# Performance work log

Hardware: AMD Instinct MI355X
Metric: run time of the kernel (lower is better)

Reference implementation:

```python
import jax, jax.numpy as jnp
import numpy as np

S_MUL, V_MUL = 32, 16          # 32x0e + 16x1o
NODE_DIM = S_MUL + 3 * V_MUL   # 80
LATENT = 128
INV_SQRT3 = 1.0 / np.sqrt(3.0)          # wigner 3j (1,1,0) / (0,1,1) / (1,0,1) factor
C_SCALAR = np.float32(1.0 / np.sqrt(48.0))   # path_norm 'element': fan into 0e = 32*1 + 16*1
C_VECTOR = np.float32(np.sqrt(3.0 / 48.0))   # irrep dim 3 / fan 48 for 1o output


def setup_inputs() -> dict:
    rng = np.random.default_rng(0)
    B, n_atoms, radius = 2048, 32, 5.0
    N = B * n_atoms
    # atoms uniform in a 10A cube -> ~300 edges per 32-atom graph at r=5
    pos_g = rng.uniform(0.0, 10.0, size=(B, n_atoms, 3)).astype(np.float32)
    diff = pos_g[:, :, None, :] - pos_g[:, None, :, :]
    d2 = (diff * diff).sum(-1)
    mask = (d2 <= radius * radius) & (d2 > 0.0)   # same predicate as build_radius_graph
    b_idx, i_idx, j_idx = np.nonzero(mask)
    edge_index = np.stack([b_idx * n_atoms + i_idx, b_idx * n_atoms + j_idx]).astype(np.int32)
    pos = pos_g.reshape(N, 3)
    z = rng.integers(0, 100, size=N).astype(np.int32)
    batch = np.repeat(np.arange(B, dtype=np.int32), n_atoms)
    L = 3  # num_layers

    def w(*shape, scale=1.0):
        return jnp.asarray((rng.standard_normal(shape) * scale).astype(np.float32))

    return dict(
        pos=jnp.asarray(pos), z=jnp.asarray(z), batch=jnp.asarray(batch),
        edge_index=jnp.asarray(edge_index), num_graphs=B,
        emb=w(100, S_MUL),                      # nn.Embedding(100, 32) ~ N(0,1)
        W_s2n=w(S_MUL, S_MUL),                  # e3nn Linear 32x0e -> 32x0e path
        W1=w(L, S_MUL, S_MUL),                  # tp path 0e x 0e -> 0e
        W2=w(L, S_MUL, V_MUL),                  # tp path 0e x 1o -> 1o
        W3=w(L, V_MUL, V_MUL),                  # tp path 1o x 0e -> 1o
        W4=w(L, V_MUL, S_MUL),                  # tp path 1o x 1o -> 0e
        Ws=w(L, S_MUL, S_MUL),                  # e3nn Linear scalar block
        Wv=w(L, V_MUL, V_MUL),                  # e3nn Linear vector block
        Wr1=w(NODE_DIM, 256, scale=1.0 / np.sqrt(NODE_DIM)), br1=jnp.zeros((256,), jnp.float32),
        Wr2=w(256, LATENT, scale=1.0 / np.sqrt(256.0)), br2=jnp.zeros((LATENT,), jnp.float32),
    )


def _forward(pos, emb, W_s2n, W1, W2, W3, W4, Ws, Wv, Wr1, br1, Wr2, br2,
             z, batch, edge_index, num_graphs):
    N = pos.shape[0]
    src, dst = edge_index[0], edge_index[1]
    # atom embedding -> node irreps (only 0e->0e path exists; vectors start at 0)
    s = (emb[z] @ W_s2n) * np.float32(1.0 / np.sqrt(S_MUL))   # (N, 32)
    v = jnp.zeros((N, V_MUL, 3), pos.dtype)                   # (N, 16, 3)
    # spherical harmonics, normalize=True, 'component': Y0 = 1, Y1 = sqrt(3) * r_hat
    rij = pos[dst] - pos[src]                                 # (E, 3)
    sh1 = np.float32(np.sqrt(3.0)) * rij / jnp.linalg.norm(rij, axis=-1, keepdims=True)
    for l in range(W1.shape[0]):
        ss, vs = s[src], v[src]                               # gather (E,32), (E,16,3)
        # FullyConnectedTensorProduct(node, sh, node), uvw weights, sh0 == 1
        m_s = C_SCALAR * (jnp.einsum('eu,uw->ew', ss, W1[l])
                          + INV_SQRT3 * jnp.einsum('eui,ei,uw->ew', vs, sh1, W4[l]))
        m_v = (C_VECTOR * INV_SQRT3) * (jnp.einsum('eu,ei,uw->ewi', ss, sh1, W2[l])
                                        + jnp.einsum('eui,uw->ewi', vs, W3[l]))
        a_s = jax.ops.segment_sum(m_s, dst, num_segments=N)   # index_add_ scatter
        a_v = jax.ops.segment_sum(m_v, dst, num_segments=N)
        # e3nn Linear (per-irrep block, 1/sqrt(fan_in)) then relu on FULL feature (as in source)
        h_s = jax.nn.relu((a_s @ Ws[l]) * np.float32(1.0 / np.sqrt(S_MUL)))
        h_v = jax.nn.relu(jnp.einsum('nvi,vw->nwi', a_v, Wv[l]) * np.float32(1.0 / np.sqrt(V_MUL)))
        s, v = s + h_s, v + h_v                               # residual
    x = jnp.concatenate([s, v.reshape(N, V_MUL * 3)], axis=-1)  # (N, 80)
    hg = jax.ops.segment_sum(x, batch, num_segments=num_graphs) # sum-pool per graph
    return jax.nn.relu(hg @ Wr1 + br1) @ Wr2 + br2              # (B, latent)


def reference(pos, emb, W_s2n, W1, W2, W3, W4, Ws, Wv, Wr1, br1, Wr2, br2,
              z, batch, edge_index, num_graphs):
    return _forward(pos, emb, W_s2n, W1, W2, W3, W4, Ws, Wv, Wr1, br1, Wr2, br2,
                    z, batch, edge_index, num_graphs)
```

## Files before the change

### kernel.cpp

```cpp
#include <hip/hip_runtime.h>
#include <math.h>

typedef __attribute__((ext_vector_type(8))) short bf16x8;
typedef __attribute__((ext_vector_type(4))) float f32x4;

#define SQRT3F     1.7320508075688772f
#define SCALE_T    0.17677669529663687f
#define SCALE_M1   0.025515518153991442f
#define SCALE_M2   0.014731391274719739f
#define SCALE_M34  0.036084391824351615f

#define FSTR 40
#define ASTR 72

__device__ __forceinline__ ushort f2bf(float f) {
    union { float f; unsigned u; } v; v.f = f;
    unsigned u = v.u;
    return (ushort)((u + 0x7FFFu + ((u >> 16) & 1u)) >> 16);
}
__device__ __forceinline__ float bf2f(ushort h) {
    union { unsigned u; float f; } v; v.u = ((unsigned)h) << 16;
    return v.f;
}
__device__ __forceinline__ f32x4 mfma(bf16x8 a, bf16x8 b, f32x4 c) {
    return __builtin_amdgcn_mfma_f32_16x16x32_bf16(a, b, c, 0, 0, 0);
}
__device__ __forceinline__ void storeAgg(ushort* AG, f32x4 t, int u0, int n) {
    uint2 u;
    u.x = f2bf(t[0]) | ((unsigned)f2bf(t[1]) << 16);
    u.y = f2bf(t[2]) | ((unsigned)f2bf(t[3]) << 16);
    *(uint2*)&AG[n*ASTR + u0] = u;
}
__device__ __forceinline__ void rmw4(ushort* F, int c, int n0, f32x4 h) {
    uint2* p = (uint2*)&F[c*FSTR + n0];
    uint2 o = *p;
    float f0 = bf2f((ushort)(o.x      )) + fmaxf(h[0], 0.f);
    float f1 = bf2f((ushort)(o.x >> 16)) + fmaxf(h[1], 0.f);
    float f2 = bf2f((ushort)(o.y      )) + fmaxf(h[2], 0.f);
    float f3 = bf2f((ushort)(o.y >> 16)) + fmaxf(h[3], 0.f);
    uint2 w;
    w.x = f2bf(f0) | ((unsigned)f2bf(f1) << 16);
    w.y = f2bf(f2) | ((unsigned)f2bf(f3) << 16);
    *p = w;
}

__global__ void prep_kernel(const float* __restrict__ emb,
                            const float* __restrict__ W_s2n,
                            const float* __restrict__ W1, const float* __restrict__ W2,
                            const float* __restrict__ W3, const float* __restrict__ W4,
                            const float* __restrict__ Ws, const float* __restrict__ Wv,
                            ushort* __restrict__ Tbf, ushort* __restrict__ Mbf)
{
    int idx = blockIdx.x * blockDim.x + threadIdx.x;
    if (idx < 3200) {
        int r = idx >> 5, c = idx & 31;
        float acc = 0.f;
        for (int k = 0; k < 32; ++k) acc += emb[r*32 + k] * W_s2n[k*32 + c];
        Tbf[idx] = f2bf(acc * SCALE_T);
        return;
    }
    idx -= 3200;
    if (idx < 3*48*64) {
        int lyr = idx / 3072, rem = idx % 3072;
        int row = rem >> 6, u = rem & 63;
        float val = 0.f;
        if (row < 32) {
            int w = row;
            if (u < 32) {
                float a = 0.f;
                for (int k = 0; k < 32; ++k)
                    a += W1[lyr*1024 + u*32 + k] * Ws[lyr*1024 + k*32 + w];
                val = a * SCALE_M1;
            } else if (u < 48) {
                int uu = u - 32; float a = 0.f;
                for (int k = 0; k < 32; ++k)
                    a += W4[lyr*512 + uu*32 + k] * Ws[lyr*1024 + k*32 + w];
                val = a * SCALE_M2;
            }
        } else {
            int w = row - 32;
            if (u < 32) {
                float a = 0.f;
                for (int k = 0; k < 16; ++k)
                    a += W2[lyr*512 + u*16 + k] * Wv[lyr*256 + k*16 + w];
                val = a * SCALE_M34;
            } else if (u < 48) {
                int uu = u - 32; float a = 0.f;
                for (int k = 0; k < 16; ++k)
                    a += W3[lyr*256 + uu*16 + k] * Wv[lyr*256 + k*16 + w];
                val = a * SCALE_M34;
            }
        }
        Mbf[lyr*3072 + row*64 + u] = f2bf(val);
    }
}

__global__ __launch_bounds__(256)
void gnn_kernel(const float* __restrict__ pos, const int* __restrict__ z,
                const ushort* __restrict__ Tbf, const ushort* __restrict__ Mbf,
                const float* __restrict__ Wr1, const float* __restrict__ br1,
                const float* __restrict__ Wr2, const float* __restrict__ br2,
                float* __restrict__ out, int B)
{
    __shared__ __align__(16) char smem[45312];
    ushort* featA = (ushort*)smem;
    ushort* aggA  = (ushort*)(smem + 25600);
    float*  hgl   = (float*)(smem + 44032);
    float*  h1    = (float*)aggA;
    float*  red   = ((float*)aggA) + 1024;

    const int tid = threadIdx.x;
    const int wv = tid >> 6, l = tid & 63;
    const int g  = blockIdx.x*4 + wv;
    ushort* F  = featA + wv*80*FSTR;
    ushort* AG = aggA  + wv*32*ASTR;

    for (int i = l; i < 32*(ASTR/2); i += 64) ((uint*)AG)[i] = 0;
    for (int i = l; i < 48*(FSTR/2); i += 64) ((uint*)(F + 32*FSTR))[i] = 0;

    {
        int n = l & 31, h = l >> 5;
        int zg = z[g*32 + n];
        uint4 t0 = *(const uint4*)(Tbf + zg*32 + h*16);
        uint4 t1 = *(const uint4*)(Tbf + zg*32 + h*16 + 8);
        unsigned ua[8] = {t0.x, t0.y, t0.z, t0.w, t1.x, t1.y, t1.z, t1.w};
        #pragma unroll
        for (int q = 0; q < 8; ++q) {
            F[(h*16 + 2*q    )*FSTR + n] = (ushort)ua[q];
            F[(h*16 + 2*q + 1)*FSTR + n] = (ushort)(ua[q] >> 16);
        }
    }

    const int ln = l & 15, kq = l >> 4;
    bf16x8 adjf[4][2];
    {
        const int k0 = kq*8;
        #pragma unroll
        for (int nt = 0; nt < 2; ++nt) {
            int ng = g*32 + nt*16 + ln;
            float px = pos[3*ng], py = pos[3*ng+1], pz = pos[3*ng+2];
            union { bf16x8 v; ushort s[8]; } o[4];
            #pragma unroll
            for (int jj = 0; jj < 8; ++jj) {
                int j = g*32 + k0 + jj;
                float dx = __fsub_rn(px, pos[3*j]);
                float dy = __fsub_rn(py, pos[3*j+1]);
                float dz = __fsub_rn(pz, pos[3*j+2]);
                float d2 = __fadd_rn(__fadd_rn(__fmul_rn(dx,dx), __fmul_rn(dy,dy)),
                                     __fmul_rn(dz,dz));
                bool on = (d2 <= 25.0f) && (d2 > 0.0f);
                float rinv = on ? rsqrtf(d2) * SQRT3F : 0.f;
                o[0].s[jj] = on ? (ushort)0x3F80 : (ushort)0;
                o[1].s[jj] = f2bf(dx * rinv);
                o[2].s[jj] = f2bf(dy * rinv);
                o[3].s[jj] = f2bf(dz * rinv);
            }
            #pragma unroll
            for (int w = 0; w < 4; ++w) adjf[w][nt] = o[w].v;
        }
    }

    const f32x4 z4 = {0.f, 0.f, 0.f, 0.f};

    for (int lay = 0; lay < 3; ++lay) {
        const ushort* Mg = Mbf + lay*3072;
        bf16x8 fs0 = *(const bf16x8*)&F[(     ln)*FSTR + kq*8];
        bf16x8 fs1 = *(const bf16x8*)&F[(16 + ln)*FSTR + kq*8];
        bf16x8 fv0 = *(const bf16x8*)&F[(32 + ln)*FSTR + kq*8];
        bf16x8 fv1 = *(const bf16x8*)&F[(48 + ln)*FSTR + kq*8];
        bf16x8 fv2 = *(const bf16x8*)&F[(64 + ln)*FSTR + kq*8];
        bf16x8 bmS0[2], bmS1[2], bmV[2];
        #pragma unroll
        for (int kc = 0; kc < 2; ++kc) {
            bmS0[kc] = *(const bf16x8*)&Mg[(     ln)*64 + kc*32 + kq*8];
            bmS1[kc] = *(const bf16x8*)&Mg[(16 + ln)*64 + kc*32 + kq*8];
            bmV [kc] = *(const bf16x8*)&Mg[(32 + ln)*64 + kc*32 + kq*8];
        }

        #pragma unroll
        for (int nt = 0; nt < 2; ++nt) {
            f32x4 t;
            t = mfma(fs0, adjf[0][nt], z4);
            storeAgg(AG, t,      kq*4, nt*16 + ln);
            t = mfma(fs1, adjf[0][nt], z4);
            storeAgg(AG, t, 16 + kq*4, nt*16 + ln);
            t = mfma(fv2, adjf[3][nt], z4);
            t = mfma(fv1, adjf[2][nt], t);
            t = mfma(fv0, adjf[1][nt], t);
            storeAgg(AG, t, 32 + kq*4, nt*16 + ln);
        }
        f32x4 hs[2][2] = {{z4, z4}, {z4, z4}};
        #pragma unroll
        for (int kc = 0; kc < 2; ++kc)
            #pragma unroll
            for (int mt = 0; mt < 2; ++mt) {
                bf16x8 ag = *(const bf16x8*)&AG[(mt*16 + ln)*ASTR + kc*32 + kq*8];
                hs[mt][0] = mfma(ag, bmS0[kc], hs[mt][0]);
                hs[mt][1] = mfma(ag, bmS1[kc], hs[mt][1]);
            }
        #pragma unroll
        for (int mt = 0; mt < 2; ++mt)
            #pragma unroll
            for (int wt = 0; wt < 2; ++wt)
                rmw4(F, wt*16 + ln, mt*16 + kq*4, hs[mt][wt]);

        #pragma unroll
        for (int i = 0; i < 3; ++i) {
            bf16x8 fvi = (i == 0) ? fv0 : (i == 1) ? fv1 : fv2;
            #pragma unroll
            for (int nt = 0; nt < 2; ++nt) {
                f32x4 t;
                t = mfma(fs0, adjf[1+i][nt], z4);
                storeAgg(AG, t,      kq*4, nt*16 + ln);
                t = mfma(fs1, adjf[1+i][nt], z4);
                storeAgg(AG, t, 16 + kq*4, nt*16 + ln);
                t = mfma(fvi, adjf[0][nt], z4);
                storeAgg(AG, t, 32 + kq*4, nt*16 + ln);
            }
            f32x4 hv[2] = {z4, z4};
            #pragma unroll
            for (int kc = 0; kc < 2; ++kc)
                #pragma unroll
                for (int mt = 0; mt < 2; ++mt) {
                    bf16x8 ag = *(const bf16x8*)&AG[(mt*16 + ln)*ASTR + kc*32 + kq*8];
                    hv[mt] = mfma(ag, bmV[kc], hv[mt]);
                }
            #pragma unroll
            for (int mt = 0; mt < 2; ++mt)
                rmw4(F, 32 + i*16 + ln, mt*16 + kq*4, hv[mt]);
        }
    }

    for (int f = l; f < 80; f += 64) {
        const ushort* row;
        if (f < 32) row = &F[f*FSTR];
        else { int c = f - 32, w = c/3, i = c - 3*w; row = &F[(32 + i*16 + w)*FSTR]; }
        const uint* r32 = (const uint*)row;
        float acc = 0.f;
        #pragma unroll
        for (int q = 0; q < 16; ++q) {
            uint u = r32[q];
            acc += bf2f((ushort)u) + bf2f((ushort)(u >> 16));
        }
        hgl[wv*80 + f] = acc;
    }
    __syncthreads();

    {
        const int w = tid;
        float acc0 = br1[w];
        float acc1 = acc0, acc2 = acc0, acc3 = acc0;
        #pragma unroll 4
        for (int f = 0; f < 80; ++f) {
            float wvv = Wr1[f*256 + w];
            acc0 = fmaf(hgl[0*80 + f], wvv, acc0);
            acc1 = fmaf(hgl[1*80 + f], wvv, acc1);
            acc2 = fmaf(hgl[2*80 + f], wvv, acc2);
            acc3 = fmaf(hgl[3*80 + f], wvv, acc3);
        }
        h1[0*256 + w] = fmaxf(acc0, 0.f);
        h1[1*256 + w] = fmaxf(acc1, 0.f);
        h1[2*256 + w] = fmaxf(acc2, 0.f);
        h1[3*256 + w] = fmaxf(acc3, 0.f);
    }
    __syncthreads();
    {
        const int g0 = blockIdx.x * 4;
        const int w2 = tid & 127, kh = tid >> 7;
        const float4* h1v = (const float4*)h1;
        float s0 = 0.f, s1 = 0.f, s2 = 0.f, s3 = 0.f;
        #pragma unroll 2
        for (int k4 = kh*32; k4 < kh*32 + 32; ++k4) {
            float4 hA = h1v[0*64 + k4];
            float4 hB = h1v[1*64 + k4];
            float4 hC = h1v[2*64 + k4];
            float4 hD = h1v[3*64 + k4];
            int k = k4 * 4;
            float m0 = Wr2[(size_t)(k+0)*128 + w2];
            float m1 = Wr2[(size_t)(k+1)*128 + w2];
            float m2 = Wr2[(size_t)(k+2)*128 + w2];
            float m3 = Wr2[(size_t)(k+3)*128 + w2];
            s0 = fmaf(hA.x,m0, fmaf(hA.y,m1, fmaf(hA.z,m2, fmaf(hA.w,m3, s0))));
            s1 = fmaf(hB.x,m0, fmaf(hB.y,m1, fmaf(hB.z,m2, fmaf(hB.w,m3, s1))));
            s2 = fmaf(hC.x,m0, fmaf(hC.y,m1, fmaf(hC.z,m2, fmaf(hC.w,m3, s2))));
            s3 = fmaf(hD.x,m0, fmaf(hD.y,m1, fmaf(hD.z,m2, fmaf(hD.w,m3, s3))));
        }
        if (kh) {
            red[0*128 + w2] = s0; red[1*128 + w2] = s1;
            red[2*128 + w2] = s2; red[3*128 + w2] = s3;
        }
        __syncthreads();
        if (!kh) {
            float b = br2[w2];
            out[(size_t)(g0+0)*128 + w2] = s0 + red[0*128 + w2] + b;
            out[(size_t)(g0+1)*128 + w2] = s1 + red[1*128 + w2] + b;
            out[(size_t)(g0+2)*128 + w2] = s2 + red[2*128 + w2] + b;
            out[(size_t)(g0+3)*128 + w2] = s3 + red[3*128 + w2] + b;
        }
    }
}

extern "C" void kernel_launch(void* const* d_in, const int* in_sizes, int n_in,
                              void* d_out, int out_size, void* d_ws, size_t ws_size,
                              hipStream_t stream)
{
    const float* pos   = (const float*)d_in[0];
    const int*   z     = (const int*)d_in[1];
    const float* emb   = (const float*)d_in[5];
    const float* W_s2n = (const float*)d_in[6];
    const float* W1    = (const float*)d_in[7];
    const float* W2    = (const float*)d_in[8];
    const float* W3    = (const float*)d_in[9];
    const float* W4    = (const float*)d_in[10];
    const float* Ws    = (const float*)d_in[11];
    const float* Wv    = (const float*)d_in[12];
    const float* Wr1   = (const float*)d_in[13];
    const float* br1   = (const float*)d_in[14];
    const float* Wr2   = (const float*)d_in[15];
    const float* br2   = (const float*)d_in[16];
    float* out = (float*)d_out;

    const int B = out_size / 128;

    char* p = (char*)d_ws;
    ushort* Tbf = (ushort*)p;  p += 6400;
    ushort* Mbf = (ushort*)p;  p += 18432;

    const int prep_total = 3200 + 3*48*64;
    prep_kernel<<<(prep_total + 255) / 256, 256, 0, stream>>>(
        emb, W_s2n, W1, W2, W3, W4, Ws, Wv, Tbf, Mbf);

    gnn_kernel<<<B / 4, 256, 0, stream>>>(pos, z, Tbf, Mbf,
                                          Wr1, br1, Wr2, br2, out, B);
}
```

Baseline: 115.7 us.

## Split each graph across two wavefronts by node-row tile, two graphs per block

Each graph is now processed by two wavefronts, each owning one 16-row node tile, instead of one wavefront doing both tiles. Blocks hold two graphs, so twice as many blocks launch, and shared memory per block is halved with a launch bound of four blocks. The goal is more parallelism and occupancy and shorter per-wave serial MFMA chains. The cost is block-wide barriers each layer to share features between the two waves, and the readout MLP now amortises Wr1/Wr2 loads over only two graphs.

New measurement: 116.4 us. Within noise of the previous version (+0.6%).

```diff
diff --git a/kernel.cpp b/kernel.cpp
--- a/kernel.cpp
+++ b/kernel.cpp
@@ -95,70 +95,68 @@
     }
 }
 
-__global__ __launch_bounds__(256)
+__global__ __launch_bounds__(256, 4)
 void gnn_kernel(const float* __restrict__ pos, const int* __restrict__ z,
                 const ushort* __restrict__ Tbf, const ushort* __restrict__ Mbf,
                 const float* __restrict__ Wr1, const float* __restrict__ br1,
                 const float* __restrict__ Wr2, const float* __restrict__ br2,
                 float* __restrict__ out, int B)
 {
-    __shared__ __align__(16) char smem[45312];
+    __shared__ __align__(16) char smem[22656];
     ushort* featA = (ushort*)smem;
-    ushort* aggA  = (ushort*)(smem + 25600);
-    float*  hgl   = (float*)(smem + 44032);
+    ushort* aggA  = (ushort*)(smem + 12800);
+    float*  hgl   = (float*)(smem + 22016);
     float*  h1    = (float*)aggA;
-    float*  red   = ((float*)aggA) + 1024;
 
     const int tid = threadIdx.x;
     const int wv = tid >> 6, l = tid & 63;
-    const int g  = blockIdx.x*4 + wv;
-    ushort* F  = featA + wv*80*FSTR;
-    ushort* AG = aggA  + wv*32*ASTR;
-
-    for (int i = l; i < 32*(ASTR/2); i += 64) ((uint*)AG)[i] = 0;
-    for (int i = l; i < 48*(FSTR/2); i += 64) ((uint*)(F + 32*FSTR))[i] = 0;
-
+    const int gw = wv >> 1;
+    const int mt = wv & 1;
+    const int g  = blockIdx.x*2 + gw;
+    ushort* F  = featA + gw*80*FSTR;
+    ushort* AG = aggA  + wv*16*ASTR;
+
+    for (int i = l; i < 16*(ASTR/2); i += 64) ((uint*)AG)[i] = 0;
     {
-        int n = l & 31, h = l >> 5;
+        const int t2 = tid & 127;
+        for (int i = t2; i < 48*(FSTR/2); i += 128) ((uint*)(F + 32*FSTR))[i] = 0;
+        int n = t2 & 31, h = t2 >> 5;
         int zg = z[g*32 + n];
-        uint4 t0 = *(const uint4*)(Tbf + zg*32 + h*16);
-        uint4 t1 = *(const uint4*)(Tbf + zg*32 + h*16 + 8);
-        unsigned ua[8] = {t0.x, t0.y, t0.z, t0.w, t1.x, t1.y, t1.z, t1.w};
-        #pragma unroll
-        for (int q = 0; q < 8; ++q) {
-            F[(h*16 + 2*q    )*FSTR + n] = (ushort)ua[q];
-            F[(h*16 + 2*q + 1)*FSTR + n] = (ushort)(ua[q] >> 16);
+        uint4 t0 = *(const uint4*)(Tbf + zg*32 + h*8);
+        unsigned ua[4] = {t0.x, t0.y, t0.z, t0.w};
+        #pragma unroll
+        for (int q = 0; q < 4; ++q) {
+            F[(h*8 + 2*q    )*FSTR + n] = (ushort)ua[q];
+            F[(h*8 + 2*q + 1)*FSTR + n] = (ushort)(ua[q] >> 16);
         }
     }
 
     const int ln = l & 15, kq = l >> 4;
-    bf16x8 adjf[4][2];
+    bf16x8 adjf[4];
     {
         const int k0 = kq*8;
-        #pragma unroll
-        for (int nt = 0; nt < 2; ++nt) {
-            int ng = g*32 + nt*16 + ln;
-            float px = pos[3*ng], py = pos[3*ng+1], pz = pos[3*ng+2];
-            union { bf16x8 v; ushort s[8]; } o[4];
-            #pragma unroll
-            for (int jj = 0; jj < 8; ++jj) {
-                int j = g*32 + k0 + jj;
-                float dx = __fsub_rn(px, pos[3*j]);
-                float dy = __fsub_rn(py, pos[3*j+1]);
-                float dz = __fsub_rn(pz, pos[3*j+2]);
-                float d2 = __fadd_rn(__fadd_rn(__fmul_rn(dx,dx), __fmul_rn(dy,dy)),
-                                     __fmul_rn(dz,dz));
-                bool on = (d2 <= 25.0f) && (d2 > 0.0f);
-                float rinv = on ? rsqrtf(d2) * SQRT3F : 0.f;
-                o[0].s[jj] = on ? (ushort)0x3F80 : (ushort)0;
-                o[1].s[jj] = f2bf(dx * rinv);
-                o[2].s[jj] = f2bf(dy * rinv);
-                o[3].s[jj] = f2bf(dz * rinv);
-            }
-            #pragma unroll
-            for (int w = 0; w < 4; ++w) adjf[w][nt] = o[w].v;
-        }
-    }
+        int ng = g*32 + mt*16 + ln;
+        float px = pos[3*ng], py = pos[3*ng+1], pz = pos[3*ng+2];
+        union { bf16x8 v; ushort s[8]; } o[4];
+        #pragma unroll
+        for (int jj = 0; jj < 8; ++jj) {
+            int j = g*32 + k0 + jj;
+            float dx = __fsub_rn(px, pos[3*j]);
+            float dy = __fsub_rn(py, pos[3*j+1]);
+            float dz = __fsub_rn(pz, pos[3*j+2]);
+            float d2 = __fadd_rn(__fadd_rn(__fmul_rn(dx,dx), __fmul_rn(dy,dy)),
+                                 __fmul_rn(dz,dz));
+            bool on = (d2 <= 25.0f) && (d2 > 0.0f);
+            float rinv = on ? rsqrtf(d2) * SQRT3F : 0.f;
+            o[0].s[jj] = on ? (ushort)0x3F80 : (ushort)0;
+            o[1].s[jj] = f2bf(dx * rinv);
+            o[2].s[jj] = f2bf(dy * rinv);
+            o[3].s[jj] = f2bf(dz * rinv);
+        }
+        #pragma unroll
+        for (int w = 0; w < 4; ++w) adjf[w] = o[w].v;
+    }
+    __syncthreads();
 
     const f32x4 z4 = {0.f, 0.f, 0.f, 0.f};
 
@@ -176,65 +174,59 @@
             bmS1[kc] = *(const bf16x8*)&Mg[(16 + ln)*64 + kc*32 + kq*8];
             bmV [kc] = *(const bf16x8*)&Mg[(32 + ln)*64 + kc*32 + kq*8];
         }
-
-        #pragma unroll
-        for (int nt = 0; nt < 2; ++nt) {
+        __syncthreads();
+
+        {
             f32x4 t;
-            t = mfma(fs0, adjf[0][nt], z4);
-            storeAgg(AG, t,      kq*4, nt*16 + ln);
-            t = mfma(fs1, adjf[0][nt], z4);
-            storeAgg(AG, t, 16 + kq*4, nt*16 + ln);
-            t = mfma(fv2, adjf[3][nt], z4);
-            t = mfma(fv1, adjf[2][nt], t);
-            t = mfma(fv0, adjf[1][nt], t);
-            storeAgg(AG, t, 32 + kq*4, nt*16 + ln);
-        }
-        f32x4 hs[2][2] = {{z4, z4}, {z4, z4}};
-        #pragma unroll
-        for (int kc = 0; kc < 2; ++kc)
-            #pragma unroll
-            for (int mt = 0; mt < 2; ++mt) {
-                bf16x8 ag = *(const bf16x8*)&AG[(mt*16 + ln)*ASTR + kc*32 + kq*8];
-                hs[mt][0] = mfma(ag, bmS0[kc], hs[mt][0]);
-                hs[mt][1] = mfma(ag, bmS1[kc], hs[mt][1]);
-            }
-        #pragma unroll
-        for (int mt = 0; mt < 2; ++mt)
-            #pragma unroll
-            for (int wt = 0; wt < 2; ++wt)
-                rmw4(F, wt*16 + ln, mt*16 + kq*4, hs[mt][wt]);
+            t = mfma(fs0, adjf[0], z4);
+            storeAgg(AG, t,      kq*4, ln);
+            t = mfma(fs1, adjf[0], z4);
+            storeAgg(AG, t, 16 + kq*4, ln);
+            t = mfma(fv2, adjf[3], z4);
+            t = mfma(fv1, adjf[2], t);
+            t = mfma(fv0, adjf[1], t);
+            storeAgg(AG, t, 32 + kq*4, ln);
+        }
+        f32x4 hs[2] = {z4, z4};
+        #pragma unroll
+        for (int kc = 0; kc < 2; ++kc) {
+            bf16x8 ag = *(const bf16x8*)&AG[ln*ASTR + kc*32 + kq*8];
+            hs[0] = mfma(ag, bmS0[kc], hs[0]);
+            hs[1] = mfma(ag, bmS1[kc], hs[1]);
+        }
+        #pragma unroll
+        for (int wt = 0; wt < 2; ++wt)
+            rmw4(F, wt*16 + ln, mt*16 + kq*4, hs[wt]);
 
         #pragma unroll
         for (int i = 0; i < 3; ++i) {
             bf16x8 fvi = (i == 0) ? fv0 : (i == 1) ? fv1 : fv2;
+            {
+                f32x4 t;
+                t = mfma(fs0, adjf[1+i], z4);
+                storeAgg(AG, t,      kq*4, ln);
+                t = mfma(fs1, adjf[1+i], z4);
+                storeAgg(AG, t, 16 + kq*4, ln);
+                t = mfma(fvi, adjf[0], z4);
+                storeAgg(AG, t, 32 + kq*4, ln);
+            }
+            f32x4 hv = z4;
             #pragma unroll
-            for (int nt = 0; nt < 2; ++nt) {
-                f32x4 t;
-                t = mfma(fs0, adjf[1+i][nt], z4);
-                storeAgg(AG, t,      kq*4, nt*16 + ln);
-                t = mfma(fs1, adjf[1+i][nt], z4);
-                storeAgg(AG, t, 16 + kq*4, nt*16 + ln);
-                t = mfma(fvi, adjf[0][nt], z4);
-                storeAgg(AG, t, 32 + kq*4, nt*16 + ln);
+            for (int kc = 0; kc < 2; ++kc) {
+                bf16x8 ag = *(const bf16x8*)&AG[ln*ASTR + kc*32 + kq*8];
+                hv = mfma(ag, bmV[kc], hv);
             }
-            f32x4 hv[2] = {z4, z4};
-            #pragma unroll
-            for (int kc = 0; kc < 2; ++kc)
-                #pragma unroll
-                for (int mt = 0; mt < 2; ++mt) {
-                    bf16x8 ag = *(const bf16x8*)&AG[(mt*16 + ln)*ASTR + kc*32 + kq*8];
-                    hv[mt] = mfma(ag, bmV[kc], hv[mt]);
-                }
-            #pragma unroll
-            for (int mt = 0; mt < 2; ++mt)
-                rmw4(F, 32 + i*16 + ln, mt*16 + kq*4, hv[mt]);
-        }
-    }
-
-    for (int f = l; f < 80; f += 64) {
+            rmw4(F, 32 + i*16 + ln, mt*16 + kq*4, hv);
+        }
+        __syncthreads();
+    }
+
+    if (tid < 160) {
+        int pg = tid / 80, f = tid - pg*80;
         const ushort* row;
-        if (f < 32) row = &F[f*FSTR];
-        else { int c = f - 32, w = c/3, i = c - 3*w; row = &F[(32 + i*16 + w)*FSTR]; }
+        ushort* Fp = featA + pg*80*FSTR;
+        if (f < 32) row = &Fp[f*FSTR];
+        else { int c = f - 32, w = c/3, i = c - 3*w; row = &Fp[(32 + i*16 + w)*FSTR]; }
         const uint* r32 = (const uint*)row;
         float acc = 0.f;
         #pragma unroll
@@ -242,61 +234,39 @@
             uint u = r32[q];
             acc += bf2f((ushort)u) + bf2f((ushort)(u >> 16));
         }
-        hgl[wv*80 + f] = acc;
+        hgl[pg*80 + f] = acc;
     }
     __syncthreads();
 
     {
         const int w = tid;
         float acc0 = br1[w];
-        float acc1 = acc0, acc2 = acc0, acc3 = acc0;
+        float acc1 = acc0;
         #pragma unroll 4
         for (int f = 0; f < 80; ++f) {
             float wvv = Wr1[f*256 + w];
             acc0 = fmaf(hgl[0*80 + f], wvv, acc0);
             acc1 = fmaf(hgl[1*80 + f], wvv, acc1);
-            acc2 = fmaf(hgl[2*80 + f], wvv, acc2);
-            acc3 = fmaf(hgl[3*80 + f], wvv, acc3);
         }
         h1[0*256 + w] = fmaxf(acc0, 0.f);
         h1[1*256 + w] = fmaxf(acc1, 0.f);
-        h1[2*256 + w] = fmaxf(acc2, 0.f);
-        h1[3*256 + w] = fmaxf(acc3, 0.f);
     }
     __syncthreads();
     {
-        const int g0 = blockIdx.x * 4;
-        const int w2 = tid & 127, kh = tid >> 7;
-        const float4* h1v = (const float4*)h1;
-        float s0 = 0.f, s1 = 0.f, s2 = 0.f, s3 = 0.f;
-        #pragma unroll 2
-        for (int k4 = kh*32; k4 < kh*32 + 32; ++k4) {
-            float4 hA = h1v[0*64 + k4];
-            float4 hB = h1v[1*64 + k4];
-            float4 hC = h1v[2*64 + k4];
-            float4 hD = h1v[3*64 + k4];
+        const int pg = tid >> 7, w2 = tid & 127;
+        const float4* h1v = (const float4*)(h1 + pg*256);
+        float s = 0.f;
+        #pragma unroll 4
+        for (int k4 = 0; k4 < 64; ++k4) {
+            float4 hA = h1v[k4];
             int k = k4 * 4;
             float m0 = Wr2[(size_t)(k+0)*128 + w2];
             float m1 = Wr2[(size_t)(k+1)*128 + w2];
             float m2 = Wr2[(size_t)(k+2)*128 + w2];
             float m3 = Wr2[(size_t)(k+3)*128 + w2];
-            s0 = fmaf(hA.x,m0, fmaf(hA.y,m1, fmaf(hA.z,m2, fmaf(hA.w,m3, s0))));
-            s1 = fmaf(hB.x,m0, fmaf(hB.y,m1, fmaf(hB.z,m2, fmaf(hB.w,m3, s1))));
-            s2 = fmaf(hC.x,m0, fmaf(hC.y,m1, fmaf(hC.z,m2, fmaf(hC.w,m3, s2))));
-            s3 = fmaf(hD.x,m0, fmaf(hD.y,m1, fmaf(hD.z,m2, fmaf(hD.w,m3, s3))));
-        }
-        if (kh) {
-            red[0*128 + w2] = s0; red[1*128 + w2] = s1;
-            red[2*128 + w2] = s2; red[3*128 + w2] = s3;
-        }
-        __syncthreads();
-        if (!kh) {
-            float b = br2[w2];
-            out[(size_t)(g0+0)*128 + w2] = s0 + red[0*128 + w2] + b;
-            out[(size_t)(g0+1)*128 + w2] = s1 + red[1*128 + w2] + b;
-            out[(size_t)(g0+2)*128 + w2] = s2 + red[2*128 + w2] + b;
-            out[(size_t)(g0+3)*128 + w2] = s3 + red[3*128 + w2] + b;
-        }
+            s = fmaf(hA.x,m0, fmaf(hA.y,m1, fmaf(hA.z,m2, fmaf(hA.w,m3, s))));
+        }
+        out[(size_t)(blockIdx.x*2 + pg)*128 + w2] = s + br2[w2];
     }
 }
 
@@ -330,6 +300,6 @@
     prep_kernel<<<(prep_total + 255) / 256, 256, 0, stream>>>(
         emb, W_s2n, W1, W2, W3, W4, Ws, Wv, Tbf, Mbf);
 
-    gnn_kernel<<<B / 4, 256, 0, stream>>>(pos, z, Tbf, Mbf,
+    gnn_kernel<<<B / 2, 256, 0, stream>>>(pos, z, Tbf, Mbf,
                                           Wr1, br1, Wr2, br2, out, B);
 }
```
